# Performance work log

Measured on AMD Instinct MI355X. Metric: run time of the kernel, lower is better.

The kernel has to match this reference:

```python
import jax, jax.numpy as jnp
import numpy as np

N, E, D = 50000, 1600000, 3     # nodes, edges, pseudo-coordinate dim
IN_F, OUT_F = 32, 32
KS = 4                           # kernel size per dim (open spline)
K = KS ** D                      # 64 kernel weight matrices
S = 2 ** D                       # (degree+1)^D basis combos for degree-1 splines


def setup_inputs() -> dict:
    key = jax.random.key(0)
    k1, k2, k3, k4, k5 = jax.random.split(key, 5)
    features = jax.random.normal(k1, (N, IN_F), jnp.float32)
    pseudo = jax.random.uniform(k2, (E, D), jnp.float32)      # normalized edge attrs in [0,1]
    stdv = 1.0 / np.sqrt(IN_F * K)
    weight = jax.random.uniform(k3, (K, IN_F, OUT_F), jnp.float32, -stdv, stdv)
    bias = jax.random.uniform(k4, (OUT_F,), jnp.float32, -stdv, stdv)
    edge_index = jax.random.randint(k5, (2, E), 0, N, jnp.int32)
    return {"features": features, "pseudo": pseudo, "weight": weight,
            "bias": bias, "edge_index": edge_index}


def _spline_basis(pseudo):
    """Degree-1 open B-spline basis. Returns (w [S,E], flat_idx [S,E])."""
    v = pseudo * (KS - 1)                                   # open-spline scaling
    bot = jnp.clip(jnp.floor(v), 0, KS - 2).astype(jnp.int32)   # [E,D]
    frac = v - bot.astype(v.dtype)                          # [E,D] in [0,1]
    bits = (jnp.arange(S)[:, None] >> jnp.arange(D)[None, :]) & 1   # [S,D]
    idx = bot[None, :, :] + bits[:, None, :]                # [S,E,D] in [0,KS-1]
    w = jnp.where(bits[:, None, :] == 1, frac[None], 1.0 - frac[None]).prod(-1)  # [S,E]
    strides = (KS ** jnp.arange(D)).astype(jnp.int32)
    flat = (idx * strides).sum(-1)                          # [S,E] in [0,K-1]
    return w, flat


def reference(features, pseudo, weight, bias, edge_index):
    row, col = edge_index[0], edge_index[1]                 # target, source
    w, flat = _spline_basis(pseudo)
    # Pre-transform features by every kernel weight matrix: [N,K,OUT]
    Z = jnp.einsum('ni,kio->nko', features, weight)
    # Per-edge message: sum over the S active basis functions (irregular gather)
    msg = jnp.zeros((E, OUT_F), Z.dtype)
    for s in range(S):                                      # S=8, fixed small loop
        msg = msg + w[s][:, None] * Z[col, flat[s]]
    # Scatter-mean to target nodes
    out = jax.ops.segment_sum(msg, row, num_segments=N)
    deg = jax.ops.segment_sum(jnp.ones((E,), features.dtype), row, num_segments=N)
    return out / jnp.maximum(deg, 1.0)[:, None] + bias
```

## Files before the change

### kernel.cpp

```cpp
#include <hip/hip_runtime.h>
#include <hip/hip_bf16.h>

#define NN 50000
#define EE 1600000
#define BPB 96
#define CH 1024
#define NCHUNK ((EE + CH - 1) / CH)
#define GG 128
#define GSZ (EE / GG)
#define NRB 196

typedef __attribute__((ext_vector_type(8))) short    s16x8;
typedef __attribute__((ext_vector_type(4))) float    f32x4;
typedef __attribute__((ext_vector_type(2))) unsigned u32x2;
typedef __attribute__((ext_vector_type(4))) unsigned u32x4;

static __device__ __forceinline__ short f2bs(float x) {
  __hip_bfloat16 h = __float2bfloat16(x);
  short s; __builtin_memcpy(&s, &h, 2); return s;
}

__constant__ int kOffs[8] = {0, 1, 4, 5, 16, 17, 20, 21};

__global__ __launch_bounds__(256) void group_rank(const int* __restrict__ ei,
                                                  unsigned short* __restrict__ lrank,
                                                  int* __restrict__ gcnt) {
  __shared__ unsigned lh32[NN / 2];
  for (int j = threadIdx.x; j < NN / 2; j += 256) lh32[j] = 0;
  __syncthreads();
  const int g  = blockIdx.x;
  const int e0 = g * GSZ;
  for (int i = threadIdx.x; i < GSZ; i += 256) {
    int e = e0 + i;
    int row = ei[e];
    unsigned add = (row & 1) ? 0x10000u : 1u;
    unsigned ret = atomicAdd(&lh32[row >> 1], add);
    unsigned r = (row & 1) ? (ret >> 16) : (ret & 0xFFFFu);
    lrank[e] = (unsigned short)r;
  }
  __syncthreads();
  for (int j = threadIdx.x; j < NN / 2; j += 256) {
    unsigned u = lh32[j];
    gcnt[(size_t)g * NN + 2 * j]     = (int)(u & 0xFFFFu);
    gcnt[(size_t)g * NN + 2 * j + 1] = (int)(u >> 16);
  }
}

#define PREP_BLOCKS (160 + NCHUNK)
__global__ __launch_bounds__(256) void prep(const float* __restrict__ W,
                                            const float* __restrict__ f,
                                            const float* __restrict__ pseudo,
                                            short* __restrict__ Wb,
                                            short* __restrict__ fbh,
                                            int* __restrict__ bh) {
  const int b = blockIdx.x;
  if (b < 32) {
    int tid = b * 256 + threadIdx.x;
    int t = tid >> 6, l = tid & 63;
    int c = t * 16 + (l & 15);
    int k0 = (l >> 4) * 8;
    s16x8 frag;
#pragma unroll
    for (int j = 0; j < 8; ++j)
      frag[j] = f2bs(W[(c >> 5) * 1024 + (k0 + j) * 32 + (c & 31)]);
    ((s16x8*)Wb)[tid] = frag;
  } else if (b < 160) {
    for (int tid = (b - 32) * 256 + threadIdx.x; tid < NN * 32 / 8; tid += 128 * 256) {
      const f32x4* fp = (const f32x4*)f + (size_t)tid * 2;
      f32x4 a = fp[0], c = fp[1];
      s16x8 o;
#pragma unroll
      for (int j = 0; j < 4; ++j) { o[j] = f2bs(a[j]); o[4 + j] = f2bs(c[j]); }
      ((s16x8*)fbh)[tid] = o;
    }
  } else {
    __shared__ int lh[27];
    if (threadIdx.x < 27) lh[threadIdx.x] = 0;
    __syncthreads();
    const int c  = b - 160;
    const int e0 = c * CH;
#pragma unroll
    for (int i = 0; i < CH / 256; ++i) {
      int e = e0 + i * 256 + threadIdx.x;
      if (e < EE) {
        float v0 = pseudo[e * 3 + 0] * 3.0f;
        float v1 = pseudo[e * 3 + 1] * 3.0f;
        float v2 = pseudo[e * 3 + 2] * 3.0f;
        int b0 = (int)fminf(fmaxf(floorf(v0), 0.0f), 2.0f);
        int b1 = (int)fminf(fmaxf(floorf(v1), 0.0f), 2.0f);
        int b2 = (int)fminf(fmaxf(floorf(v2), 0.0f), 2.0f);
        atomicAdd(&lh[b0 + 3 * b1 + 9 * b2], 1);
      }
    }
    __syncthreads();
    if (threadIdx.x < 27) bh[threadIdx.x * NCHUNK + c] = lh[threadIdx.x];
  }
}

__global__ __launch_bounds__(256) void sum_p1(const int* __restrict__ gcnt,
                                              const int* __restrict__ bh,
                                              int* __restrict__ degi,
                                              int* __restrict__ rpart,
                                              int* __restrict__ btot) {
  const int b = blockIdx.x;
  const int lane = threadIdx.x & 63;
  const int wid  = threadIdx.x >> 6;
  __shared__ int ws[4];
  if (b < NRB) {
    int row = b * 256 + threadIdx.x;
    int s = 0;
    if (row < NN) {
#pragma unroll 8
      for (int g = 0; g < GG; ++g) s += gcnt[(size_t)g * NN + row];
      degi[row] = s;
    }
    int x = s;
#pragma unroll
    for (int d = 1; d < 64; d <<= 1) x += __shfl_xor(x, d, 64);
    if (lane == 0) ws[wid] = x;
    __syncthreads();
    if (threadIdx.x == 0) rpart[b] = ws[0] + ws[1] + ws[2] + ws[3];
  } else {
    int q = b - NRB;
    if (q >= 27) return;
    int s = 0;
    for (int c = threadIdx.x; c < NCHUNK; c += 256) s += bh[q * NCHUNK + c];
    int x = s;
#pragma unroll
    for (int d = 1; d < 64; d <<= 1) x += __shfl_xor(x, d, 64);
    if (lane == 0) ws[wid] = x;
    __syncthreads();
    if (threadIdx.x == 0) btot[q] = ws[0] + ws[1] + ws[2] + ws[3];
  }
}

__global__ __launch_bounds__(256) void scan_tiny(const int* __restrict__ rpart,
                                                 const int* __restrict__ btot,
                                                 int* __restrict__ rpartx,
                                                 int* __restrict__ bstart) {
  __shared__ int sA[256];
  __shared__ int sB[32];
  const int t = threadIdx.x;
  int origA = (t < NRB) ? rpart[t] : 0;
  sA[t] = origA;
  int origB = 0;
  if (t < 32) { origB = (t < 27) ? btot[t] : 0; sB[t] = origB; }
  __syncthreads();
#pragma unroll
  for (int d = 1; d < 256; d <<= 1) {
    int a = (t >= d) ? sA[t - d] : 0;
    int bb = (t < 32 && d < 32 && t >= d) ? sB[t - d] : 0;
    __syncthreads();
    sA[t] += a;
    if (t < 32 && d < 32) sB[t] += bb;
    __syncthreads();
  }
  if (t < NRB) rpartx[t] = sA[t] - origA;
  if (t < 27)  bstart[t] = sB[t] - origB;
  if (t == 27) bstart[27] = EE;
}

__global__ __launch_bounds__(256) void scan_p3(int* __restrict__ bh,
                                               const int* __restrict__ degi,
                                               const int* __restrict__ rpartx,
                                               const int* __restrict__ bstart,
                                               int* __restrict__ rstart) {
  const int b = blockIdx.x;
  const int lane = threadIdx.x & 63;
  const int wid  = threadIdx.x >> 6;
  __shared__ int wsum[4];
  __shared__ int ctot;
  if (b < NRB) {
    int row = b * 256 + threadIdx.x;
    int v = (row < NN) ? degi[row] : 0;
    int x = v;
#pragma unroll
    for (int d = 1; d < 64; d <<= 1) {
      int y = __shfl_up(x, d, 64);
      if (lane >= d) x += y;
    }
    if (lane == 63) wsum[wid] = x;
    __syncthreads();
    int off = 0;
#pragma unroll
    for (int w = 0; w < 4; ++w) if (w < wid) off += wsum[w];
    if (row < NN) rstart[row] = rpartx[b] + off + (x - v);
    if (b == 0 && threadIdx.x == 0) rstart[NN] = EE;
  } else {
    int q = b - NRB;
    if (q >= 27) return;
    int carry = bstart[q];
    for (int c0 = 0; c0 < NCHUNK; c0 += 256) {
      int c = c0 + threadIdx.x;
      int v = (c < NCHUNK) ? bh[q * NCHUNK + c] : 0;
      int x = v;
#pragma unroll
      for (int d = 1; d < 64; d <<= 1) {
        int y = __shfl_up(x, d, 64);
        if (lane >= d) x += y;
      }
      if (lane == 63) wsum[wid] = x;
      __syncthreads();
      int off = 0;
#pragma unroll
      for (int w = 0; w < 4; ++w) if (w < wid) off += wsum[w];
      if (c < NCHUNK) bh[q * NCHUNK + c] = carry + off + (x - v);
      __syncthreads();
      if (threadIdx.x == 0) ctot = wsum[0] + wsum[1] + wsum[2] + wsum[3];
      __syncthreads();
      carry += ctot;
    }
  }
}

__global__ __launch_bounds__(256) void group_base(int* __restrict__ gcnt,
                                                  const int* __restrict__ rstart) {
  int row = blockIdx.x * 256 + threadIdx.x;
  if (row >= NN) return;
  int run = rstart[row];
  for (int g0 = 0; g0 < GG; g0 += 8) {
    int t[8];
#pragma unroll
    for (int j = 0; j < 8; ++j) t[j] = gcnt[(size_t)(g0 + j) * NN + row];
#pragma unroll
    for (int j = 0; j < 8; ++j) {
      int v = t[j];
      gcnt[(size_t)(g0 + j) * NN + row] = run;
      run += v;
    }
  }
}

static __device__ __forceinline__ unsigned q16(float fr) {
  return min((unsigned)(fr * 65536.0f), 65535u);
}
__global__ __launch_bounds__(256) void bucket_scatter(const float* __restrict__ pseudo,
                                                      const int* __restrict__ ei,
                                                      const unsigned short* __restrict__ lrank,
                                                      const int* __restrict__ gcnt,
                                                      const int* __restrict__ bh,
                                                      u32x2* __restrict__ edata,
                                                      int* __restrict__ rpos_arr) {
  __shared__ int lh[27];
  __shared__ int bb[27];
  if (threadIdx.x < 27) {
    lh[threadIdx.x] = 0;
    bb[threadIdx.x] = bh[threadIdx.x * NCHUNK + blockIdx.x];
  }
  __syncthreads();
  const int e0 = blockIdx.x * CH;
#pragma unroll
  for (int i = 0; i < CH / 256; ++i) {
    int e = e0 + i * 256 + threadIdx.x;
    if (e < EE) {
      float v0 = pseudo[e * 3 + 0] * 3.0f;
      float v1 = pseudo[e * 3 + 1] * 3.0f;
      float v2 = pseudo[e * 3 + 2] * 3.0f;
      float fb0 = fmaxf(fminf(floorf(v0), 2.0f), 0.0f);
      float fb1 = fmaxf(fminf(floorf(v1), 2.0f), 0.0f);
      float fb2 = fmaxf(fminf(floorf(v2), 2.0f), 0.0f);
      int q = (int)fb0 + 3 * (int)fb1 + 9 * (int)fb2;
      int rk = atomicAdd(&lh[q], 1);
      int pos = bb[q] + rk;
      int row = ei[e];
      int col = ei[EE + e];
      int ge  = e / GSZ;
      u32x2 pk;
      pk.x = q16(v0 - fb0) | (q16(v1 - fb1) << 16);
      pk.y = q16(v2 - fb2) | ((unsigned)col << 16);
      edata[pos] = pk;
      rpos_arr[pos] = gcnt[(size_t)ge * NN + row] + (int)lrank[e];
    }
  }
}

__global__ __launch_bounds__(256) void edge_mfma_nw(const u32x2* __restrict__ edata,
                                                    const int* __restrict__ rpos_arr,
                                                    const short* __restrict__ fbh,
                                                    const short* __restrict__ Wb,
                                                    const int* __restrict__ bstart,
                                                    u32x4* __restrict__ msg4) {
  const int q   = blockIdx.x / BPB;
  const int sub = blockIdx.x % BPB;
  const int l   = threadIdx.x & 63;
  const int wid = threadIdx.x >> 6;

  const int start = bstart[q];
  const int end   = bstart[q + 1];
  const int nE    = end - start;
  if (nE <= 0) return;
  const int ngroups = (nE + 15) >> 4;

  const int b0 = q % 3, b1 = (q / 3) % 3, b2 = q / 9;
  const int base = b0 + 4 * b1 + 16 * b2;
  const int ko[8] = {0, 1, 4, 5, 16, 17, 20, 21};

  s16x8 bf[8][2];
#pragma unroll
  for (int s = 0; s < 8; ++s) {
    int kmat = base + ko[s];
#pragma unroll
    for (int oh = 0; oh < 2; ++oh)
      bf[s][oh] = ((const s16x8*)Wb)[(kmat * 2 + oh) * 64 + l];
  }

  const int m   = l & 15;
  const int kq  = l >> 4;
  const int stride = BPB * 4;
  const float inv16 = 1.0f / 65536.0f;

  int gA = sub * 4 + wid;
  if (gA >= ngroups) return;
  int gB = gA + stride;

  int iA = start + gA * 16 + m;  int ciA = iA < end ? iA : start;
  int iB = start + gB * 16 + m;  int ciB = (gB < ngroups && iB < end) ? iB : start;

  u32x2 edA = edata[ciA];  int rpA = rpos_arr[ciA];
  u32x2 edB = edata[ciB];  int rpB = rpos_arr[ciB];
  s16x8 afA = ((const s16x8*)fbh)[(size_t)(edA.y >> 16) * 4 + kq];

  while (true) {
    const bool moreB = gB < ngroups;
    const int gC = gB + stride;
    int iC = start + gC * 16 + m;
    int ciC = (gC < ngroups && iC < end) ? iC : start;
    u32x2 edC = edata[ciC];
    int   rpC = rpos_arr[ciC];
    s16x8 afB = ((const s16x8*)fbh)[(size_t)(edB.y >> 16) * 4 + kq];

    float f0 = (float)(edA.x & 0xFFFFu) * inv16;
    float f1 = (float)(edA.x >> 16)     * inv16;
    float f2 = (float)(edA.y & 0xFFFFu) * inv16;
    float g0 = 1.0f - f0, g1c = 1.0f - f1, g2c = 1.0f - f2;
    float w8[8];
    w8[0] = g0 * g1c * g2c; w8[1] = f0 * g1c * g2c;
    w8[2] = g0 * f1 * g2c;  w8[3] = f0 * f1 * g2c;
    w8[4] = g0 * g1c * f2;  w8[5] = f0 * g1c * f2;
    w8[6] = g0 * f1 * f2;   w8[7] = f0 * f1 * f2;

    f32x4 acc0 = {0.f, 0.f, 0.f, 0.f}, acc1 = {0.f, 0.f, 0.f, 0.f};
#pragma unroll
    for (int s = 0; s < 8; ++s) {
      f32x4 d0 = __builtin_amdgcn_mfma_f32_16x16x32_bf16(bf[s][0], afA,
                   (f32x4){0.f, 0.f, 0.f, 0.f}, 0, 0, 0);
      f32x4 d1 = __builtin_amdgcn_mfma_f32_16x16x32_bf16(bf[s][1], afA,
                   (f32x4){0.f, 0.f, 0.f, 0.f}, 0, 0, 0);
      float ws = w8[s];
#pragma unroll
      for (int r = 0; r < 4; ++r) {
        acc0[r] += ws * d0[r];
        acc1[r] += ws * d1[r];
      }
    }

    if (gA * 16 + m < nE) {
      u32x4 pk;
      pk.x = (unsigned)(unsigned short)f2bs(acc0[0]) |
             ((unsigned)(unsigned short)f2bs(acc1[0]) << 16);
      pk.y = (unsigned)(unsigned short)f2bs(acc0[1]) |
             ((unsigned)(unsigned short)f2bs(acc1[1]) << 16);
      pk.z = (unsigned)(unsigned short)f2bs(acc0[2]) |
             ((unsigned)(unsigned short)f2bs(acc1[2]) << 16);
      pk.w = (unsigned)(unsigned short)f2bs(acc0[3]) |
             ((unsigned)(unsigned short)f2bs(acc1[3]) << 16);
      msg4[(size_t)rpA * 4 + kq] = pk;
    }

    if (!moreB) break;
    gA = gB; edA = edB; rpA = rpB; afA = afB;
    gB = gC; edB = edC; rpB = rpC;
  }
}

__global__ __launch_bounds__(256) void gather_out(const unsigned* __restrict__ msg,
                                                  const int* __restrict__ rstart,
                                                  const float* __restrict__ bias,
                                                  float* __restrict__ out) {
  int n = (blockIdx.x * 256 + threadIdx.x) >> 4;
  int j = threadIdx.x & 15;
  if (n >= NN) return;
  int s = rstart[n], e = rstart[n + 1];
  int cnt = e - s;
  const unsigned* mp = msg + (size_t)s * 16 + j;
  float s0 = 0.f, s1 = 0.f;
  int i = 0;
  for (; i + 4 <= cnt; i += 4) {
    unsigned uA = mp[(size_t)(i + 0) * 16];
    unsigned uB = mp[(size_t)(i + 1) * 16];
    unsigned uC = mp[(size_t)(i + 2) * 16];
    unsigned uD = mp[(size_t)(i + 3) * 16];
    s0 += __uint_as_float(uA << 16); s1 += __uint_as_float(uA & 0xFFFF0000u);
    s0 += __uint_as_float(uB << 16); s1 += __uint_as_float(uB & 0xFFFF0000u);
    s0 += __uint_as_float(uC << 16); s1 += __uint_as_float(uC & 0xFFFF0000u);
    s0 += __uint_as_float(uD << 16); s1 += __uint_as_float(uD & 0xFFFF0000u);
  }
  for (; i < cnt; ++i) {
    unsigned u = mp[(size_t)i * 16];
    s0 += __uint_as_float(u << 16);
    s1 += __uint_as_float(u & 0xFFFF0000u);
  }
  float d = fmaxf((float)cnt, 1.0f);
  out[n * 32 + j]      = s0 / d + bias[j];
  out[n * 32 + 16 + j] = s1 / d + bias[16 + j];
}

static __device__ __forceinline__ void spline_basis(const float* __restrict__ pseudo,
                                                    int e, float w[8], int& base) {
  float v0 = pseudo[e * 3 + 0] * 3.0f;
  float v1 = pseudo[e * 3 + 1] * 3.0f;
  float v2 = pseudo[e * 3 + 2] * 3.0f;
  float b0 = fmaxf(fminf(floorf(v0), 2.0f), 0.0f);
  float b1 = fmaxf(fminf(floorf(v1), 2.0f), 0.0f);
  float b2 = fmaxf(fminf(floorf(v2), 2.0f), 0.0f);
  float f0 = v0 - b0, f1 = v1 - b1, f2 = v2 - b2;
  float g0 = 1.0f - f0, g1 = 1.0f - f1, g2 = 1.0f - f2;
  base = (int)b0 + 4 * (int)b1 + 16 * (int)b2;
  w[0] = g0 * g1 * g2; w[1] = f0 * g1 * g2;
  w[2] = g0 * f1 * g2; w[3] = f0 * f1 * g2;
  w[4] = g0 * g1 * f2; w[5] = f0 * g1 * f2;
  w[6] = g0 * f1 * f2; w[7] = f0 * f1 * f2;
}

__global__ __launch_bounds__(256) void edge_direct(const float* __restrict__ pseudo,
                                                   const int* __restrict__ ei,
                                                   const float* __restrict__ f,
                                                   const float* __restrict__ W,
                                                   float* __restrict__ acc,
                                                   float* __restrict__ deg) {
  const int tid = blockIdx.x * 256 + threadIdx.x;
  const int e = tid >> 5;
  const int o = tid & 31;
  if (e >= EE) return;
  const int row = ei[e];
  const int col = ei[EE + e];
  float w[8]; int base;
  spline_basis(pseudo, e, w, base);
  const float myf = f[col * 32 + o];
  float a = 0.0f;
  for (int i = 0; i < 32; ++i) {
    float fi = __shfl(myf, i, 32);
    float wsum = 0.0f;
#pragma unroll
    for (int s = 0; s < 8; ++s)
      wsum += w[s] * W[(size_t)(base + kOffs[s]) * 1024 + i * 32 + o];
    a += fi * wsum;
  }
  atomicAdd(acc + (size_t)row * 32 + o, a);
  if (o == 0) atomicAdd(deg + row, 1.0f);
}

__global__ __launch_bounds__(256) void finalize(const float* __restrict__ acc,
                                                const float* __restrict__ deg,
                                                const float* __restrict__ bias,
                                                float* __restrict__ out) {
  int tid = blockIdx.x * 256 + threadIdx.x;
  if (tid >= NN * 32) return;
  int n = tid >> 5, o = tid & 31;
  float d = fmaxf(deg[n], 1.0f);
  out[tid] = acc[tid] / d + bias[o];
}

extern "C" void kernel_launch(void* const* d_in, const int* in_sizes, int n_in,
                              void* d_out, int out_size, void* d_ws, size_t ws_size,
                              hipStream_t stream) {
  const float* f      = (const float*)d_in[0];
  const float* pseudo = (const float*)d_in[1];
  const float* W      = (const float*)d_in[2];
  const float* bias   = (const float*)d_in[3];
  const int*   ei     = (const int*)d_in[4];
  float* out = (float*)d_out;

  constexpr size_t DEGI_OFF   = 0;
  constexpr size_t RPART_OFF  = 200064;
  constexpr size_t BTOT_OFF   = 200960;
  constexpr size_t RPARTX_OFF = 201088;
  constexpr size_t BST_OFF    = 201984;
  constexpr size_t RST_OFF    = 202112;
  constexpr size_t BH_OFF     = 402176;
  constexpr size_t LRANK_OFF  = 571008;
  constexpr size_t GCNT_OFF   = LRANK_OFF + (size_t)EE * 2;
  constexpr size_t ED_OFF     = GCNT_OFF + (size_t)GG * NN * 4;
  constexpr size_t RPOS_OFF   = ED_OFF + (size_t)EE * 8;
  constexpr size_t MSG_OFF    = RPOS_OFF + (size_t)EE * 4;
  constexpr size_t FBH_OFF    = MSG_OFF + (size_t)EE * 64;
  constexpr size_t WB_OFF     = FBH_OFF + (size_t)NN * 64;
  constexpr size_t TOTAL      = WB_OFF + 128 * 64 * 8 * 2;

  char* ws = (char*)d_ws;

  if (ws_size >= TOTAL) {
    int*            degi   = (int*)(ws + DEGI_OFF);
    int*            rpart  = (int*)(ws + RPART_OFF);
    int*            btot   = (int*)(ws + BTOT_OFF);
    int*            rpartx = (int*)(ws + RPARTX_OFF);
    int*            bst    = (int*)(ws + BST_OFF);
    int*            rst    = (int*)(ws + RST_OFF);
    int*            bh     = (int*)(ws + BH_OFF);
    unsigned short* lrank  = (unsigned short*)(ws + LRANK_OFF);
    int*            gcnt   = (int*)(ws + GCNT_OFF);
    u32x2*          edata  = (u32x2*)(ws + ED_OFF);
    int*            rpos   = (int*)(ws + RPOS_OFF);
    u32x4*          msg4   = (u32x4*)(ws + MSG_OFF);
    unsigned*       msg    = (unsigned*)(ws + MSG_OFF);
    short*          fbh    = (short*)(ws + FBH_OFF);
    short*          Wb     = (short*)(ws + WB_OFF);

    group_rank<<<GG, 256, 0, stream>>>(ei, lrank, gcnt);
    prep<<<PREP_BLOCKS, 256, 0, stream>>>(W, f, pseudo, Wb, fbh, bh);
    sum_p1<<<NRB + 27, 256, 0, stream>>>(gcnt, bh, degi, rpart, btot);
    scan_tiny<<<1, 256, 0, stream>>>(rpart, btot, rpartx, bst);
    scan_p3<<<NRB + 27, 256, 0, stream>>>(bh, degi, rpartx, bst, rst);
    group_base<<<(NN + 255) / 256, 256, 0, stream>>>(gcnt, rst);
    bucket_scatter<<<NCHUNK, 256, 0, stream>>>(pseudo, ei, lrank, gcnt, bh, edata, rpos);
    edge_mfma_nw<<<27 * BPB, 256, 0, stream>>>(edata, rpos, fbh, Wb, bst, msg4);
    gather_out<<<(NN * 16 + 255) / 256, 256, 0, stream>>>(msg, rst, bias, out);
  } else {
    constexpr size_t ACC_SZ = (size_t)NN * 32 * 4;
    float* acc = (float*)ws;
    float* deg = (float*)(ws + ACC_SZ);
    hipMemsetAsync(acc, 0, ACC_SZ + (size_t)NN * 4, stream);
    edge_direct<<<(EE * 32) / 256, 256, 0, stream>>>(pseudo, ei, f, W, acc, deg);
    finalize<<<(NN * 32) / 256, 256, 0, stream>>>(acc, deg, bias, out);
  }
}
```

Baseline: 252.4 us.

## Fuse tiny scan, scan pass and group-base kernels into one launch

```diff
diff --git a/kernel.cpp b/kernel.cpp
--- a/kernel.cpp
+++ b/kernel.cpp
@@ -22,15 +22,15 @@
 
 __constant__ int kOffs[8] = {0, 1, 4, 5, 16, 17, 20, 21};
 
-__global__ __launch_bounds__(256) void group_rank(const int* __restrict__ ei,
+__global__ __launch_bounds__(512) void group_rank(const int* __restrict__ ei,
                                                   unsigned short* __restrict__ lrank,
                                                   int* __restrict__ gcnt) {
   __shared__ unsigned lh32[NN / 2];
-  for (int j = threadIdx.x; j < NN / 2; j += 256) lh32[j] = 0;
+  for (int j = threadIdx.x; j < NN / 2; j += 512) lh32[j] = 0;
   __syncthreads();
   const int g  = blockIdx.x;
   const int e0 = g * GSZ;
-  for (int i = threadIdx.x; i < GSZ; i += 256) {
+  for (int i = threadIdx.x; i < GSZ; i += 512) {
     int e = e0 + i;
     int row = ei[e];
     unsigned add = (row & 1) ? 0x10000u : 1u;
@@ -39,7 +39,7 @@
     lrank[e] = (unsigned short)r;
   }
   __syncthreads();
-  for (int j = threadIdx.x; j < NN / 2; j += 256) {
+  for (int j = threadIdx.x; j < NN / 2; j += 512) {
     unsigned u = lh32[j];
     gcnt[(size_t)g * NN + 2 * j]     = (int)(u & 0xFFFFu);
     gcnt[(size_t)g * NN + 2 * j + 1] = (int)(u >> 16);
@@ -134,46 +134,36 @@
   }
 }
 
-__global__ __launch_bounds__(256) void scan_tiny(const int* __restrict__ rpart,
+__global__ __launch_bounds__(256) void scan_base(int* __restrict__ bh,
+                                                 const int* __restrict__ degi,
+                                                 const int* __restrict__ rpart,
                                                  const int* __restrict__ btot,
-                                                 int* __restrict__ rpartx,
+                                                 int* __restrict__ gcnt,
+                                                 int* __restrict__ rstart,
                                                  int* __restrict__ bstart) {
+  const int b = blockIdx.x;
+  const int t = threadIdx.x;
+  const int lane = t & 63;
+  const int wid  = t >> 6;
   __shared__ int sA[256];
-  __shared__ int sB[32];
-  const int t = threadIdx.x;
-  int origA = (t < NRB) ? rpart[t] : 0;
-  sA[t] = origA;
-  int origB = 0;
-  if (t < 32) { origB = (t < 27) ? btot[t] : 0; sB[t] = origB; }
-  __syncthreads();
-#pragma unroll
-  for (int d = 1; d < 256; d <<= 1) {
-    int a = (t >= d) ? sA[t - d] : 0;
-    int bb = (t < 32 && d < 32 && t >= d) ? sB[t - d] : 0;
-    __syncthreads();
-    sA[t] += a;
-    if (t < 32 && d < 32) sB[t] += bb;
-    __syncthreads();
-  }
-  if (t < NRB) rpartx[t] = sA[t] - origA;
-  if (t < 27)  bstart[t] = sB[t] - origB;
-  if (t == 27) bstart[27] = EE;
-}
-
-__global__ __launch_bounds__(256) void scan_p3(int* __restrict__ bh,
-                                               const int* __restrict__ degi,
-                                               const int* __restrict__ rpartx,
-                                               const int* __restrict__ bstart,
-                                               int* __restrict__ rstart) {
-  const int b = blockIdx.x;
-  const int lane = threadIdx.x & 63;
-  const int wid  = threadIdx.x >> 6;
+  __shared__ int sbst[28];
   __shared__ int wsum[4];
   __shared__ int ctot;
   if (b < NRB) {
-    int row = b * 256 + threadIdx.x;
-    int v = (row < NN) ? degi[row] : 0;
-    int x = v;
+    int v = (t < NRB) ? rpart[t] : 0;
+    sA[t] = v;
+    __syncthreads();
+#pragma unroll
+    for (int d = 1; d < 256; d <<= 1) {
+      int a = (t >= d) ? sA[t - d] : 0;
+      __syncthreads();
+      sA[t] += a;
+      __syncthreads();
+    }
+    int rbase = (b == 0) ? 0 : sA[b - 1];
+    int row = b * 256 + t;
+    int dv = (row < NN) ? degi[row] : 0;
+    int x = dv;
 #pragma unroll
     for (int d = 1; d < 64; d <<= 1) {
       int y = __shfl_up(x, d, 64);
@@ -184,14 +174,41 @@
     int off = 0;
 #pragma unroll
     for (int w = 0; w < 4; ++w) if (w < wid) off += wsum[w];
-    if (row < NN) rstart[row] = rpartx[b] + off + (x - v);
-    if (b == 0 && threadIdx.x == 0) rstart[NN] = EE;
+    int rv = rbase + off + (x - dv);
+    if (row < NN) rstart[row] = rv;
+    if (b == 0 && t == 0) rstart[NN] = EE;
+    if (row < NN) {
+      int run = rv;
+      for (int g0 = 0; g0 < GG; g0 += 8) {
+        int tb[8];
+#pragma unroll
+        for (int j = 0; j < 8; ++j) tb[j] = gcnt[(size_t)(g0 + j) * NN + row];
+#pragma unroll
+        for (int j = 0; j < 8; ++j) {
+          int vv = tb[j];
+          gcnt[(size_t)(g0 + j) * NN + row] = run;
+          run += vv;
+        }
+      }
+    }
   } else {
     int q = b - NRB;
-    if (q >= 27) return;
-    int carry = bstart[q];
+    if (t < 64) {
+      int v = (lane < 27) ? btot[lane] : 0;
+      int x = v;
+#pragma unroll
+      for (int d = 1; d < 32; d <<= 1) {
+        int y = __shfl_up(x, d, 64);
+        if (lane >= d) x += y;
+      }
+      if (lane < 27) sbst[lane] = x - v;
+      if (lane == 26) sbst[27] = x;
+    }
+    __syncthreads();
+    if (q == 0 && t < 28) bstart[t] = sbst[t];
+    int carry = sbst[q];
     for (int c0 = 0; c0 < NCHUNK; c0 += 256) {
-      int c = c0 + threadIdx.x;
+      int c = c0 + t;
       int v = (c < NCHUNK) ? bh[q * NCHUNK + c] : 0;
       int x = v;
 #pragma unroll
@@ -206,27 +223,9 @@
       for (int w = 0; w < 4; ++w) if (w < wid) off += wsum[w];
       if (c < NCHUNK) bh[q * NCHUNK + c] = carry + off + (x - v);
       __syncthreads();
-      if (threadIdx.x == 0) ctot = wsum[0] + wsum[1] + wsum[2] + wsum[3];
+      if (t == 0) ctot = wsum[0] + wsum[1] + wsum[2] + wsum[3];
       __syncthreads();
       carry += ctot;
-    }
-  }
-}
-
-__global__ __launch_bounds__(256) void group_base(int* __restrict__ gcnt,
-                                                  const int* __restrict__ rstart) {
-  int row = blockIdx.x * 256 + threadIdx.x;
-  if (row >= NN) return;
-  int run = rstart[row];
-  for (int g0 = 0; g0 < GG; g0 += 8) {
-    int t[8];
-#pragma unroll
-    for (int j = 0; j < 8; ++j) t[j] = gcnt[(size_t)(g0 + j) * NN + row];
-#pragma unroll
-    for (int j = 0; j < 8; ++j) {
-      int v = t[j];
-      gcnt[(size_t)(g0 + j) * NN + row] = run;
-      run += v;
     }
   }
 }
@@ -474,7 +473,6 @@
   constexpr size_t DEGI_OFF   = 0;
   constexpr size_t RPART_OFF  = 200064;
   constexpr size_t BTOT_OFF   = 200960;
-  constexpr size_t RPARTX_OFF = 201088;
   constexpr size_t BST_OFF    = 201984;
   constexpr size_t RST_OFF    = 202112;
   constexpr size_t BH_OFF     = 402176;
@@ -493,7 +491,6 @@
     int*            degi   = (int*)(ws + DEGI_OFF);
     int*            rpart  = (int*)(ws + RPART_OFF);
     int*            btot   = (int*)(ws + BTOT_OFF);
-    int*            rpartx = (int*)(ws + RPARTX_OFF);
     int*            bst    = (int*)(ws + BST_OFF);
     int*            rst    = (int*)(ws + RST_OFF);
     int*            bh     = (int*)(ws + BH_OFF);
@@ -506,12 +503,10 @@
     short*          fbh    = (short*)(ws + FBH_OFF);
     short*          Wb     = (short*)(ws + WB_OFF);
 
-    group_rank<<<GG, 256, 0, stream>>>(ei, lrank, gcnt);
+    group_rank<<<GG, 512, 0, stream>>>(ei, lrank, gcnt);
     prep<<<PREP_BLOCKS, 256, 0, stream>>>(W, f, pseudo, Wb, fbh, bh);
     sum_p1<<<NRB + 27, 256, 0, stream>>>(gcnt, bh, degi, rpart, btot);
-    scan_tiny<<<1, 256, 0, stream>>>(rpart, btot, rpartx, bst);
-    scan_p3<<<NRB + 27, 256, 0, stream>>>(bh, degi, rpartx, bst, rst);
-    group_base<<<(NN + 255) / 256, 256, 0, stream>>>(gcnt, rst);
+    scan_base<<<NRB + 27, 256, 0, stream>>>(bh, degi, rpart, btot, gcnt, rst, bst);
     bucket_scatter<<<NCHUNK, 256, 0, stream>>>(pseudo, ei, lrank, gcnt, bh, edata, rpos);
     edge_mfma_nw<<<27 * BPB, 256, 0, stream>>>(edata, rpos, fbh, Wb, bst, msg4);
     gather_out<<<(NN * 16 + 255) / 256, 256, 0, stream>>>(msg, rst, bias, out);
```

Result: faster. 228.3 us (-9.5%).
